# Optimization experiments

Hardware: AMD Instinct MI355X
Metric: run time of the kernel (lower is better)

The kernel has to match this reference:

```python
import jax, jax.numpy as jnp
import numpy as np

B, N, C = 32, 197, 768   # batch, tokens (num_patches+1), emb_dim
KW = 197                 # kw_dim = seq_len
L = 12                   # num_layers (weights shared, norms per-layer)
HID = 3072               # mlp hidden = 4*emb_dim


def layer_norm(x, g, b, eps=1e-5):
    mu = jnp.mean(x, axis=-1, keepdims=True)
    var = jnp.var(x, axis=-1, keepdims=True)
    return (x - mu) * jax.lax.rsqrt(var + eps) * g + b


def attention(x, qkv_w, fc_w, fc_b, ln_g, ln_b, fc2_w, fc2_b, num_heads):
    b, n, c = x.shape
    d = c // num_heads
    qkv = (x @ qkv_w).reshape(b, n, 3, num_heads, d)
    q = qkv[:, :, 0].transpose(0, 2, 1, 3)  # [B,H,N,d]
    k = qkv[:, :, 1].transpose(0, 2, 1, 3)
    v = qkv[:, :, 2].transpose(0, 2, 1, 3)
    scale = d ** -0.5
    attn = jnp.einsum('bhnd,bhmd->bhnm', q, k) * scale      # [B,H,N,N]
    attn = attn @ fc_w + fc_b                                # [B,H,N,KW]
    attn = layer_norm(attn, ln_g, ln_b)
    attn = jax.nn.softmax(attn, axis=-1)
    attn = attn.transpose(0, 1, 3, 2)                        # [B,H,KW,N]
    y = jnp.einsum('bhkn,bhnd->bhkd', attn, v)               # [B,H,KW,d]
    # fc2 applied along KW axis of y.transpose(-2,-1): out[b,h,n,d]
    out = jnp.einsum('bhkd,kn->bnhd', y, fc2_w) + fc2_b[None, :, None, None]
    return out.reshape(b, n, c)


def mlp(x, w1, b1, w2, b2):
    return jax.nn.gelu(x @ w1 + b1, approximate=False) @ w2 + b2


def setup_inputs() -> dict:
    key = jax.random.key(0)
    ks = jax.random.split(key, 16)
    s = 0.02
    return {
        'x': jax.random.normal(ks[0], (B, N, C), jnp.float32),
        'qkv_w': jax.random.normal(ks[1], (C, 3 * C), jnp.float32) * s,
        'fc_w': jax.random.normal(ks[2], (N, KW), jnp.float32) * s,
        'fc_b': jnp.zeros((KW,), jnp.float32),
        'attn_ln_g': jnp.ones((KW,), jnp.float32),
        'attn_ln_b': jnp.zeros((KW,), jnp.float32),
        'fc2_w': jax.random.normal(ks[3], (KW, N), jnp.float32) * s,
        'fc2_b': jnp.zeros((N,), jnp.float32),
        'mlp_w1': jax.random.normal(ks[4], (C, HID), jnp.float32) * s,
        'mlp_b1': jnp.zeros((HID,), jnp.float32),
        'mlp_w2': jax.random.normal(ks[5], (HID, C), jnp.float32) * s,
        'mlp_b2': jnp.zeros((C,), jnp.float32),
        'f_ln_g': jnp.ones((L, C), jnp.float32),
        'f_ln_b': jnp.zeros((L, C), jnp.float32),
        'g_ln_g': jnp.ones((L, C), jnp.float32),
        'g_ln_b': jnp.zeros((L, C), jnp.float32),
        'num_heads': 12,
    }


def reference(x, qkv_w, fc_w, fc_b, attn_ln_g, attn_ln_b, fc2_w, fc2_b,
              mlp_w1, mlp_b1, mlp_w2, mlp_b2, f_ln_g, f_ln_b, g_ln_g, g_ln_b,
              num_heads):
    # x -> cat([x,x]) -> reversible stack -> mean of the two halves
    x1, x2 = x, x
    n_layers = f_ln_g.shape[0]
    for i in range(n_layers):
        # y1 = x1 + f(x2); y2 = x2 + g(y1)  (PreNorm wraps f and g)
        y1 = x1 + attention(layer_norm(x2, f_ln_g[i], f_ln_b[i]),
                            qkv_w, fc_w, fc_b, attn_ln_g, attn_ln_b,
                            fc2_w, fc2_b, num_heads)
        y2 = x2 + mlp(layer_norm(y1, g_ln_g[i], g_ln_b[i]),
                      mlp_w1, mlp_b1, mlp_w2, mlp_b2)
        x1, x2 = y1, y2
    return (x1 + x2) * 0.5
```

## Files before the change

### kernel.cpp

```cpp
#include <hip/hip_runtime.h>
#include <math.h>

#define BB   32
#define NN   197
#define CC   768
#define HH   12
#define DD   64
#define KWW  197
#define HIDD 3072
#define NL   12
#define RR   (BB*NN)
#define BHH  (BB*HH)
#define NP   224

typedef __attribute__((ext_vector_type(8))) short short8;
typedef __attribute__((ext_vector_type(4))) float floatx4;
typedef __attribute__((ext_vector_type(4))) unsigned short us4;

__device__ __forceinline__ unsigned short f2bf(float f) {
    unsigned int u = __float_as_uint(f);
    u += 0x7fff + ((u >> 16) & 1);
    return (unsigned short)(u >> 16);
}

__global__ void ln768_kernel(const float* __restrict__ in, const float* __restrict__ g,
                             const float* __restrict__ be, unsigned short* __restrict__ out) {
    int row = blockIdx.x;
    const float* x = in + (size_t)row * CC;
    unsigned short* o = out + (size_t)row * CC;
    int t = threadIdx.x;
    float v0 = x[t], v1 = x[t+256], v2 = x[t+512];
    float s = v0+v1+v2;
    float q = v0*v0+v1*v1+v2*v2;
    for (int off = 1; off < 64; off <<= 1) {
        s += __shfl_xor(s, off, 64);
        q += __shfl_xor(q, off, 64);
    }
    __shared__ float sh[8];
    int wv = t >> 6, ln = t & 63;
    if (ln == 0) { sh[wv] = s; sh[4+wv] = q; }
    __syncthreads();
    s = sh[0]+sh[1]+sh[2]+sh[3];
    q = sh[4]+sh[5]+sh[6]+sh[7];
    float mu  = s * (1.0f/CC);
    float var = q * (1.0f/CC) - mu*mu;
    float rs  = rsqrtf(var + 1e-5f);
    o[t]     = f2bf((v0-mu)*rs*g[t]     + be[t]);
    o[t+256] = f2bf((v1-mu)*rs*g[t+256] + be[t+256]);
    o[t+512] = f2bf((v2-mu)*rs*g[t+512] + be[t+512]);
}

__global__ void reduce_ln(float* __restrict__ x2, const float* __restrict__ part,
                          const float* __restrict__ b2,
                          const float* __restrict__ g, const float* __restrict__ be,
                          unsigned short* __restrict__ out, int do_ln) {
    int row = blockIdx.x;
    float* xp = x2 + (size_t)row * CC;
    const float* p0 = part + (size_t)row * CC;
    const float* p1 = part + (size_t)RR*CC + (size_t)row * CC;
    int t = threadIdx.x;
    float v0 = xp[t]     + p0[t]     + p1[t]     + b2[t];
    float v1 = xp[t+256] + p0[t+256] + p1[t+256] + b2[t+256];
    float v2 = xp[t+512] + p0[t+512] + p1[t+512] + b2[t+512];
    xp[t] = v0; xp[t+256] = v1; xp[t+512] = v2;
    if (!do_ln) return;
    float s = v0+v1+v2;
    float q = v0*v0+v1*v1+v2*v2;
    for (int off = 1; off < 64; off <<= 1) {
        s += __shfl_xor(s, off, 64);
        q += __shfl_xor(q, off, 64);
    }
    __shared__ float sh[8];
    int wv = t >> 6, ln = t & 63;
    if (ln == 0) { sh[wv] = s; sh[4+wv] = q; }
    __syncthreads();
    s = sh[0]+sh[1]+sh[2]+sh[3];
    q = sh[4]+sh[5]+sh[6]+sh[7];
    float mu  = s * (1.0f/CC);
    float var = q * (1.0f/CC) - mu*mu;
    float rs  = rsqrtf(var + 1e-5f);
    unsigned short* o = out + (size_t)row * CC;
    o[t]     = f2bf((v0-mu)*rs*g[t]     + be[t]);
    o[t+256] = f2bf((v1-mu)*rs*g[t+256] + be[t+256]);
    o[t+512] = f2bf((v2-mu)*rs*g[t+512] + be[t+512]);
}

__global__ void transpose_cast(const float* __restrict__ in, unsigned short* __restrict__ out,
                               int K, int Nd, int Kpad) {
    __shared__ float tile[32][33];
    int n0 = blockIdx.x*32, k0 = blockIdx.y*32;
    int tx = threadIdx.x & 31, ty = threadIdx.x >> 5;
    #pragma unroll
    for (int i = 0; i < 4; i++) {
        int k = k0 + ty + i*8;
        tile[ty + i*8][tx] = (k < K && n0+tx < Nd) ? in[(size_t)k*Nd + n0 + tx] : 0.f;
    }
    __syncthreads();
    #pragma unroll
    for (int i = 0; i < 4; i++) {
        int n = n0 + ty + i*8;
        if (n < Nd && k0 + tx < Kpad) out[(size_t)n*Kpad + k0 + tx] = f2bf(tile[tx][ty + i*8]);
    }
}

template<int EPI, int KS>
__global__ __launch_bounds__(256) void gemm128(
    const unsigned short* __restrict__ A, const unsigned short* __restrict__ Bt,
    const float* __restrict__ bias, float* __restrict__ Cf, unsigned short* __restrict__ Cb,
    int M, int Nd, int K)
{
    __shared__ unsigned short As[128*64];
    __shared__ unsigned short Bs[128*64];
    int tid  = threadIdx.x;
    int wv   = tid >> 6, lane = tid & 63;
    int wm   = wv >> 1, wn = wv & 1;
    int quad = lane >> 4, mrow = lane & 15;
    int rl   = lane >> 3, ps = lane & 7;

    int gx   = gridDim.x;
    int nwg  = gx * gridDim.y;
    int orig = blockIdx.y * gx + blockIdx.x;
    int qq = nwg >> 3, rr = nwg & 7;
    int xcd = orig & 7, idx = orig >> 3;
    int wg  = (xcd < rr ? xcd*(qq+1) : rr*(qq+1) + (xcd-rr)*qq) + idx;
    int bm  = (wg / gx) * 128;
    int bn  = (wg % gx) * 128;

    const int Kc    = K / KS;
    const int kbase = (KS > 1) ? blockIdx.z * Kc : 0;

    floatx4 acc[4][4];
    #pragma unroll
    for (int i = 0; i < 4; i++)
        #pragma unroll
        for (int j = 0; j < 4; j++) acc[i][j] = (floatx4){0.f,0.f,0.f,0.f};

    for (int k0 = kbase; k0 < kbase + Kc; k0 += 64) {
        #pragma unroll
        for (int i = 0; i < 4; i++) {
            int r_ = wv*32 + i*8 + rl;
            int sl = ps ^ (r_ & 7);
            int gr = bm + r_; if (gr > M-1) gr = M-1;
            __builtin_amdgcn_global_load_lds(
                (const __attribute__((address_space(1))) void*)(A + (size_t)gr*K + k0 + sl*8),
                (__attribute__((address_space(3))) void*)(As + (wv*32 + i*8)*64),
                16, 0, 0);
        }
        #pragma unroll
        for (int i = 0; i < 4; i++) {
            int r_ = wv*32 + i*8 + rl;
            int sl = ps ^ (r_ & 7);
            int gr = bn + r_;
            __builtin_amdgcn_global_load_lds(
                (const __attribute__((address_space(1))) void*)(Bt + (size_t)gr*K + k0 + sl*8),
                (__attribute__((address_space(3))) void*)(Bs + (wv*32 + i*8)*64),
                16, 0, 0);
        }
        __syncthreads();
        #pragma unroll
        for (int kk = 0; kk < 2; kk++) {
            short8 af[4], bf[4];
            #pragma unroll
            for (int mi = 0; mi < 4; mi++) {
                int lr = wm*64 + mi*16 + mrow;
                af[mi] = *(const short8*)&As[lr*64 + (((kk<<2)|quad) ^ (lr & 7))*8];
            }
            #pragma unroll
            for (int ni = 0; ni < 4; ni++) {
                int lr = wn*64 + ni*16 + mrow;
                bf[ni] = *(const short8*)&Bs[lr*64 + (((kk<<2)|quad) ^ (lr & 7))*8];
            }
            #pragma unroll
            for (int mi = 0; mi < 4; mi++)
                #pragma unroll
                for (int ni = 0; ni < 4; ni++)
                    acc[mi][ni] = __builtin_amdgcn_mfma_f32_16x16x32_bf16(
                        af[mi], bf[ni], acc[mi][ni], 0, 0, 0);
        }
        __syncthreads();
    }

    float* Cfz = (EPI == 5) ? (Cf + (size_t)blockIdx.z * M * Nd) : Cf;
    #pragma unroll
    for (int mi = 0; mi < 4; mi++) {
        int row0 = bm + wm*64 + mi*16 + quad*4;
        #pragma unroll
        for (int ni = 0; ni < 4; ni++) {
            int col = bn + wn*64 + ni*16 + mrow;
            float bv = (EPI == 2) ? bias[col] : 0.f;
            #pragma unroll
            for (int r = 0; r < 4; r++) {
                int row = row0 + r;
                if (row >= M) continue;
                float v = acc[mi][ni][r] + bv;
                if (EPI == 2) {
                    v = v / (1.0f + __expf(-1.5957691216f*v*(1.0f + 0.044715f*v*v)));
                    Cb[(size_t)row*Nd + col] = f2bf(v);
                } else if (EPI == 5) {
                    Cfz[(size_t)row*Nd + col] = v;
                } else if (EPI == 4) {
                    int sel = col / CC;
                    int rem = col - sel*CC;
                    int h = rem >> 6, d = rem & 63;
                    int b = row / NN, n = row - b*NN;
                    int bh = b*HH + h;
                    unsigned short val = f2bf(v);
                    if (sel < 2)
                        Cb[((size_t)sel*BHH + bh)*NN*DD + (size_t)n*DD + d] = val;
                    else
                        Cb[(size_t)2*BHH*NN*DD + (size_t)bh*DD*NP + (size_t)d*NP + n] = val;
                }
            }
        }
    }
}

__global__ __launch_bounds__(256) void attn_score(
    const unsigned short* __restrict__ qb,
    const unsigned short* __restrict__ kb,
    const unsigned short* __restrict__ fw,
    const float* __restrict__ fbias,
    const float* __restrict__ g, const float* __restrict__ be,
    unsigned short* __restrict__ PT)
{
    int bh = blockIdx.y;
    int bm = blockIdx.x * 64;
    __shared__ unsigned short Ks[224*DD];
    __shared__ unsigned short S1s[64*NP];
    __shared__ unsigned short Bs[224*32];
    __shared__ float gls[NP], bls[NP], bbs[NP];
    int tid = threadIdx.x;
    if (tid < NP) {
        bool vc = tid < KWW;
        gls[tid] = vc ? g[tid]     : 1.f;
        bls[tid] = vc ? be[tid]    : 0.f;
        bbs[tid] = vc ? fbias[tid] : 0.f;
    }
    int wv = tid >> 6, lane = tid & 63;
    int quad = lane >> 4, mrow = lane & 15;

    {
        int lrow = lane >> 3, lko = (lane & 7) * 8;
        #pragma unroll
        for (int i = 0; i < 7; i++) {
            int r = wv*56 + i*8 + lrow;
            __builtin_amdgcn_global_load_lds(
                (const __attribute__((address_space(1))) void*)(kb + ((size_t)bh*NN + r)*DD + lko),
                (__attribute__((address_space(3))) void*)(Ks + (size_t)(wv*56 + i*8)*DD),
                16, 0, 0);
        }
    }
    int qrow = bm + wv*16 + mrow; if (qrow > NN-1) qrow = NN-1;
    short8 aq0 = *(const short8*)&qb[((size_t)bh*NN + qrow)*DD + quad*8];
    short8 aq1 = *(const short8*)&qb[((size_t)bh*NN + qrow)*DD + 32 + quad*8];
    __syncthreads();

    #pragma unroll
    for (int ni = 0; ni < 14; ni++) {
        floatx4 a = (floatx4){0.f,0.f,0.f,0.f};
        short8 bf0 = *(const short8*)&Ks[(size_t)(ni*16 + mrow)*DD + quad*8];
        short8 bf1 = *(const short8*)&Ks[(size_t)(ni*16 + mrow)*DD + 32 + quad*8];
        a = __builtin_amdgcn_mfma_f32_16x16x32_bf16(aq0, bf0, a, 0, 0, 0);
        a = __builtin_amdgcn_mfma_f32_16x16x32_bf16(aq1, bf1, a, 0, 0, 0);
        #pragma unroll
        for (int r = 0; r < 4; r++)
            S1s[(size_t)(wv*16 + quad*4 + r)*NP + ni*16 + mrow] = f2bf(a[r]*0.125f);
    }
    __syncthreads();

    floatx4 acc[14];
    #pragma unroll
    for (int j = 0; j < 14; j++) acc[j] = (floatx4){0.f,0.f,0.f,0.f};
    for (int k0 = 0; k0 < 7; k0++) {
        for (int c = wv; c < 14; c += 4) {
            int gr = c*16 + (lane >> 2); if (gr > KWW-1) gr = KWW-1;
            __builtin_amdgcn_global_load_lds(
                (const __attribute__((address_space(1))) void*)(fw + (size_t)gr*NP + k0*32 + (lane & 3)*8),
                (__attribute__((address_space(3))) void*)(Bs + (size_t)(c*16)*32),
                16, 0, 0);
        }
        __syncthreads();
        short8 af = *(const short8*)&S1s[(size_t)(wv*16 + mrow)*NP + k0*32 + quad*8];
        #pragma unroll
        for (int ni = 0; ni < 14; ni++) {
            short8 bf = *(const short8*)&Bs[(size_t)(ni*16 + mrow)*32 + quad*8];
            acc[ni] = __builtin_amdgcn_mfma_f32_16x16x32_bf16(af, bf, acc[ni], 0, 0, 0);
        }
        __syncthreads();
    }

    float s[4] = {}, q[4] = {};
    #pragma unroll
    for (int ni = 0; ni < 14; ni++) {
        int col = ni*16 + mrow;
        float cm = (col < KWW) ? 1.f : 0.f;
        #pragma unroll
        for (int r = 0; r < 4; r++) {
            float x = acc[ni][r] + bbs[col];
            acc[ni][r] = x;
            s[r] += x*cm; q[r] += x*x*cm;
        }
    }
    #pragma unroll
    for (int o = 1; o < 16; o <<= 1)
        #pragma unroll
        for (int r = 0; r < 4; r++) {
            s[r] += __shfl_xor(s[r], o, 64);
            q[r] += __shfl_xor(q[r], o, 64);
        }
    float mu[4], rs[4], mx[4];
    #pragma unroll
    for (int r = 0; r < 4; r++) {
        mu[r] = s[r] * (1.0f/KWW);
        float var = q[r] * (1.0f/KWW) - mu[r]*mu[r];
        rs[r] = rsqrtf(var + 1e-5f);
        mx[r] = -1e30f;
    }
    #pragma unroll
    for (int ni = 0; ni < 14; ni++) {
        int col = ni*16 + mrow;
        bool vc = col < KWW;
        #pragma unroll
        for (int r = 0; r < 4; r++) {
            float x = (acc[ni][r] - mu[r]) * rs[r] * gls[col] + bls[col];
            acc[ni][r] = x;
            if (vc) mx[r] = fmaxf(mx[r], x);
        }
    }
    #pragma unroll
    for (int o = 1; o < 16; o <<= 1)
        #pragma unroll
        for (int r = 0; r < 4; r++)
            mx[r] = fmaxf(mx[r], __shfl_xor(mx[r], o, 64));
    float se[4] = {};
    #pragma unroll
    for (int ni = 0; ni < 14; ni++) {
        int col = ni*16 + mrow;
        float cm = (col < KWW) ? 1.f : 0.f;
        #pragma unroll
        for (int r = 0; r < 4; r++) {
            float p = __expf(acc[ni][r] - mx[r]) * cm;
            acc[ni][r] = p;
            se[r] += p;
        }
    }
    #pragma unroll
    for (int o = 1; o < 16; o <<= 1)
        #pragma unroll
        for (int r = 0; r < 4; r++)
            se[r] += __shfl_xor(se[r], o, 64);
    unsigned short* Pb = PT + (size_t)bh*NP*NP;
    int row0 = bm + wv*16 + quad*4;
    float inv0 = 1.0f/se[0], inv1 = 1.0f/se[1], inv2 = 1.0f/se[2], inv3 = 1.0f/se[3];
    #pragma unroll
    for (int ni = 0; ni < 14; ni++) {
        int col = ni*16 + mrow;
        if (col >= KWW) continue;
        if (row0 + 3 < NN) {
            us4 o = { f2bf(acc[ni][0]*inv0), f2bf(acc[ni][1]*inv1),
                      f2bf(acc[ni][2]*inv2), f2bf(acc[ni][3]*inv3) };
            *(us4*)&Pb[(size_t)col*NP + row0] = o;
        } else {
            float invs[4] = {inv0, inv1, inv2, inv3};
            #pragma unroll
            for (int r = 0; r < 4; r++)
                if (row0 + r < NN)
                    Pb[(size_t)col*NP + row0 + r] = f2bf(acc[ni][r]*invs[r]);
        }
    }
}

__global__ __launch_bounds__(256) void attn_out2(
    const unsigned short* __restrict__ PT,
    const unsigned short* __restrict__ vT,
    const unsigned short* __restrict__ fw,
    const float* __restrict__ bias,
    float* __restrict__ x1)
{
    int dt = blockIdx.x;
    int bh = blockIdx.y; int b = bh / HH, h = bh - b*HH;
    __shared__ unsigned short yT[16*232];
    int wv = threadIdx.x >> 6, lane = threadIdx.x & 63;
    int quad = lane >> 4, mrow = lane & 15;
    const unsigned short* Pb = PT + (size_t)bh*NP*NP;
    const unsigned short* Vb = vT + (size_t)bh*DD*NP + (size_t)(dt*16)*NP;

    short8 bfv[7];
    #pragma unroll
    for (int kc = 0; kc < 7; kc++)
        bfv[kc] = *(const short8*)&Vb[(size_t)mrow*NP + kc*32 + quad*8];
    #pragma unroll
    for (int i = 0; i < 2; i++) {
        int t0 = wv + i*8, t1 = t0 + 4;
        bool v1 = t1 < 14;
        floatx4 a0 = (floatx4){0.f,0.f,0.f,0.f};
        floatx4 a1 = (floatx4){0.f,0.f,0.f,0.f};
        #pragma unroll
        for (int kc = 0; kc < 7; kc++) {
            short8 p0 = *(const short8*)&Pb[(size_t)(t0*16 + mrow)*NP + kc*32 + quad*8];
            a0 = __builtin_amdgcn_mfma_f32_16x16x32_bf16(p0, bfv[kc], a0, 0, 0, 0);
            if (v1) {
                short8 p1 = *(const short8*)&Pb[(size_t)(t1*16 + mrow)*NP + kc*32 + quad*8];
                a1 = __builtin_amdgcn_mfma_f32_16x16x32_bf16(p1, bfv[kc], a1, 0, 0, 0);
            }
        }
        us4 o0 = { f2bf(a0[0]), f2bf(a0[1]), f2bf(a0[2]), f2bf(a0[3]) };
        *(us4*)&yT[mrow*232 + t0*16 + quad*4] = o0;
        if (v1) {
            us4 o1 = { f2bf(a1[0]), f2bf(a1[1]), f2bf(a1[2]), f2bf(a1[3]) };
            *(us4*)&yT[mrow*232 + t1*16 + quad*4] = o1;
        }
    }
    __syncthreads();

    short8 yf[7];
    #pragma unroll
    for (int kc = 0; kc < 7; kc++)
        yf[kc] = *(const short8*)&yT[mrow*232 + kc*32 + quad*8];
    float* xb = x1 + (size_t)b*NN*CC + (size_t)h*DD + dt*16 + mrow;
    #pragma unroll
    for (int i = 0; i < 2; i++) {
        int n0t = wv + i*8, n1t = n0t + 4;
        bool v1 = n1t < 13;
        floatx4 a0 = (floatx4){0.f,0.f,0.f,0.f};
        floatx4 a1 = (floatx4){0.f,0.f,0.f,0.f};
        #pragma unroll
        for (int kc = 0; kc < 7; kc++) {
            short8 f0 = *(const short8*)&fw[(size_t)(n0t*16 + mrow)*NP + kc*32 + quad*8];
            a0 = __builtin_amdgcn_mfma_f32_16x16x32_bf16(f0, yf[kc], a0, 0, 0, 0);
            if (v1) {
                short8 f1 = *(const short8*)&fw[(size_t)(n1t*16 + mrow)*NP + kc*32 + quad*8];
                a1 = __builtin_amdgcn_mfma_f32_16x16x32_bf16(f1, yf[kc], a1, 0, 0, 0);
            }
        }
        #pragma unroll
        for (int r = 0; r < 4; r++) {
            int n = n0t*16 + quad*4 + r;
            if (n < NN) xb[(size_t)n*CC] += a0[r] + bias[n];
        }
        if (v1) {
            #pragma unroll
            for (int r = 0; r < 4; r++) {
                int n = n1t*16 + quad*4 + r;
                if (n < NN) xb[(size_t)n*CC] += a1[r] + bias[n];
            }
        }
    }
}

__global__ void init_kernel(const float* __restrict__ x, float* __restrict__ x1,
                            float* __restrict__ x2, int n) {
    int i = blockIdx.x*256 + threadIdx.x;
    if (i < n) { float v = x[i]; x1[i] = v; x2[i] = v; }
}
__global__ void final_kernel(const float* __restrict__ x1, const float* __restrict__ x2,
                             float* __restrict__ o, int n) {
    int i = blockIdx.x*256 + threadIdx.x;
    if (i < n) o[i] = 0.5f*(x1[i]+x2[i]);
}

extern "C" void kernel_launch(void* const* d_in, const int* in_sizes, int n_in,
                              void* d_out, int out_size, void* d_ws, size_t ws_size,
                              hipStream_t stream) {
    const float* x     = (const float*)d_in[0];
    const float* qkv_w = (const float*)d_in[1];
    const float* fc_w  = (const float*)d_in[2];
    const float* fc_b  = (const float*)d_in[3];
    const float* alng  = (const float*)d_in[4];
    const float* alnb  = (const float*)d_in[5];
    const float* fc2w  = (const float*)d_in[6];
    const float* fc2b  = (const float*)d_in[7];
    const float* w1    = (const float*)d_in[8];
    const float* b1    = (const float*)d_in[9];
    const float* w2    = (const float*)d_in[10];
    const float* b2    = (const float*)d_in[11];
    const float* flng  = (const float*)d_in[12];
    const float* flnb  = (const float*)d_in[13];
    const float* glng  = (const float*)d_in[14];
    const float* glnb  = (const float*)d_in[15];
    float* out = (float*)d_out;

    float* ws = (float*)d_ws;
    size_t off = 0;
    float* x1 = ws + off; off += (size_t)RR*CC;
    float* x2 = ws + off; off += (size_t)RR*CC;
    float* part = ws + off; off += (size_t)2*RR*CC;
    unsigned short* lnb = (unsigned short*)(ws + off); off += (size_t)RR*CC/2;
    unsigned short* qkvo = (unsigned short*)(ws + off);
    unsigned short* qb = qkvo;
    unsigned short* kb = qkvo + (size_t)BHH*NN*DD;
    unsigned short* vT = qkvo + (size_t)2*BHH*NN*DD;
    off += ((size_t)2*BHH*NN*DD + (size_t)BHH*DD*NP + 1) / 2;
    unsigned short* PT   = (unsigned short*)(ws + off); off += (size_t)BHH*NP*NP/2;
    unsigned short* hid  = (unsigned short*)(ws + off); off += (size_t)RR*HIDD/2;
    unsigned short* qkv_wt = (unsigned short*)(ws + off); off += (size_t)3*CC*CC/2;
    unsigned short* w1t    = (unsigned short*)(ws + off); off += (size_t)CC*HIDD/2;
    unsigned short* w2t    = (unsigned short*)(ws + off); off += (size_t)CC*HIDD/2;
    unsigned short* fc_wt  = (unsigned short*)(ws + off); off += (size_t)NN*NP/2 + 16;
    unsigned short* fc2_wt = (unsigned short*)(ws + off); off += (size_t)NP*NP/2 + 16;

    hipMemsetAsync(vT, 0, (size_t)BHH*DD*NP*2, stream);
    hipMemsetAsync(fc2_wt, 0, (size_t)NP*NP*2, stream);

    transpose_cast<<<dim3(72, 24), 256, 0, stream>>>(qkv_w, qkv_wt, CC, 3*CC, CC);
    transpose_cast<<<dim3(96, 24), 256, 0, stream>>>(w1, w1t, CC, HIDD, CC);
    transpose_cast<<<dim3(24, 96), 256, 0, stream>>>(w2, w2t, HIDD, CC, HIDD);
    transpose_cast<<<dim3(7, 7),   256, 0, stream>>>(fc_w,  fc_wt,  NN, KWW, NP);
    transpose_cast<<<dim3(7, 7),   256, 0, stream>>>(fc2w,  fc2_wt, KWW, NN, NP);

    const int nel = RR*CC;
    init_kernel<<<(nel+255)/256, 256, 0, stream>>>(x, x1, x2, nel);

    const int MT = (RR + 127) / 128;
    ln768_kernel<<<RR, 256, 0, stream>>>(x2, flng, flnb, lnb);
    for (int l = 0; l < NL; l++) {
        gemm128<4,1><<<dim3(3*CC/128, MT), 256, 0, stream>>>(
            lnb, qkv_wt, nullptr, nullptr, qb, RR, 3*CC, CC);
        attn_score<<<dim3(4, BHH), 256, 0, stream>>>(
            qb, kb, fc_wt, fc_b, alng, alnb, PT);
        attn_out2<<<dim3(4, BHH), 256, 0, stream>>>(PT, vT, fc2_wt, fc2b, x1);
        ln768_kernel<<<RR, 256, 0, stream>>>(x1, glng + l*CC, glnb + l*CC, lnb);
        gemm128<2,1><<<dim3(HIDD/128, MT), 256, 0, stream>>>(
            lnb, w1t, b1, nullptr, hid, RR, HIDD, CC);
        gemm128<5,2><<<dim3(CC/128, MT, 2), 256, 0, stream>>>(
            hid, w2t, nullptr, part, nullptr, RR, CC, HIDD);
        reduce_ln<<<RR, 256, 0, stream>>>(
            x2, part, b2, flng + ((l+1 < NL) ? (l+1)*CC : 0),
            flnb + ((l+1 < NL) ? (l+1)*CC : 0), lnb, (l+1 < NL) ? 1 : 0);
    }
    final_kernel<<<(nel+255)/256, 256, 0, stream>>>(x1, x2, out, nel);
}
```

Before: 3.402 ms.

## Double-buffer GEMM LDS tiles and fuse init/final elementwise kernels into LN passes

The 128x128 bf16 GEMM now keeps two LDS stages and issues global-to-LDS loads for the next K tile before running MFMAs on the current one, so memory latency can overlap with compute. LDS use doubles to 64 KB per block, which may lower occupancy. The init copy is merged with the first LayerNorm into one kernel. The final averaging is folded into the last residual reduce kernel, removing two full-tensor passes and two launches.

```diff
diff --git a/kernel.cpp b/kernel.cpp
--- a/kernel.cpp
+++ b/kernel.cpp
@@ -50,10 +50,45 @@
     o[t+512] = f2bf((v2-mu)*rs*g[t+512] + be[t+512]);
 }
 
+__global__ void init_ln(const float* __restrict__ x, float* __restrict__ x1,
+                        float* __restrict__ x2,
+                        const float* __restrict__ g, const float* __restrict__ be,
+                        unsigned short* __restrict__ out) {
+    int row = blockIdx.x;
+    const float* xp = x + (size_t)row * CC;
+    int t = threadIdx.x;
+    float v0 = xp[t], v1 = xp[t+256], v2 = xp[t+512];
+    float* a = x1 + (size_t)row * CC;
+    float* b = x2 + (size_t)row * CC;
+    a[t] = v0; a[t+256] = v1; a[t+512] = v2;
+    b[t] = v0; b[t+256] = v1; b[t+512] = v2;
+    float s = v0+v1+v2;
+    float q = v0*v0+v1*v1+v2*v2;
+    for (int off = 1; off < 64; off <<= 1) {
+        s += __shfl_xor(s, off, 64);
+        q += __shfl_xor(q, off, 64);
+    }
+    __shared__ float sh[8];
+    int wv = t >> 6, ln = t & 63;
+    if (ln == 0) { sh[wv] = s; sh[4+wv] = q; }
+    __syncthreads();
+    s = sh[0]+sh[1]+sh[2]+sh[3];
+    q = sh[4]+sh[5]+sh[6]+sh[7];
+    float mu  = s * (1.0f/CC);
+    float var = q * (1.0f/CC) - mu*mu;
+    float rs  = rsqrtf(var + 1e-5f);
+    unsigned short* o = out + (size_t)row * CC;
+    o[t]     = f2bf((v0-mu)*rs*g[t]     + be[t]);
+    o[t+256] = f2bf((v1-mu)*rs*g[t+256] + be[t+256]);
+    o[t+512] = f2bf((v2-mu)*rs*g[t+512] + be[t+512]);
+}
+
 __global__ void reduce_ln(float* __restrict__ x2, const float* __restrict__ part,
                           const float* __restrict__ b2,
                           const float* __restrict__ g, const float* __restrict__ be,
-                          unsigned short* __restrict__ out, int do_ln) {
+                          unsigned short* __restrict__ out,
+                          const float* __restrict__ x1f, float* __restrict__ outf,
+                          int mode) {
     int row = blockIdx.x;
     float* xp = x2 + (size_t)row * CC;
     const float* p0 = part + (size_t)row * CC;
@@ -63,7 +98,14 @@
     float v1 = xp[t+256] + p0[t+256] + p1[t+256] + b2[t+256];
     float v2 = xp[t+512] + p0[t+512] + p1[t+512] + b2[t+512];
     xp[t] = v0; xp[t+256] = v1; xp[t+512] = v2;
-    if (!do_ln) return;
+    if (mode == 2) {
+        const float* xo = x1f + (size_t)row * CC;
+        float* o = outf + (size_t)row * CC;
+        o[t]     = 0.5f*(xo[t]     + v0);
+        o[t+256] = 0.5f*(xo[t+256] + v1);
+        o[t+512] = 0.5f*(xo[t+512] + v2);
+        return;
+    }
     float s = v0+v1+v2;
     float q = v0*v0+v1*v1+v2*v2;
     for (int off = 1; off < 64; off <<= 1) {
@@ -109,8 +151,8 @@
     const float* __restrict__ bias, float* __restrict__ Cf, unsigned short* __restrict__ Cb,
     int M, int Nd, int K)
 {
-    __shared__ unsigned short As[128*64];
-    __shared__ unsigned short Bs[128*64];
+    __shared__ unsigned short As[2*128*64];
+    __shared__ unsigned short Bs[2*128*64];
     int tid  = threadIdx.x;
     int wv   = tid >> 6, lane = tid & 63;
     int wm   = wv >> 1, wn = wv & 1;
@@ -128,6 +170,7 @@
 
     const int Kc    = K / KS;
     const int kbase = (KS > 1) ? blockIdx.z * Kc : 0;
+    const int nt    = Kc / 64;
 
     floatx4 acc[4][4];
     #pragma unroll
@@ -135,40 +178,49 @@
         #pragma unroll
         for (int j = 0; j < 4; j++) acc[i][j] = (floatx4){0.f,0.f,0.f,0.f};
 
-    for (int k0 = kbase; k0 < kbase + Kc; k0 += 64) {
-        #pragma unroll
-        for (int i = 0; i < 4; i++) {
-            int r_ = wv*32 + i*8 + rl;
-            int sl = ps ^ (r_ & 7);
-            int gr = bm + r_; if (gr > M-1) gr = M-1;
-            __builtin_amdgcn_global_load_lds(
-                (const __attribute__((address_space(1))) void*)(A + (size_t)gr*K + k0 + sl*8),
-                (__attribute__((address_space(3))) void*)(As + (wv*32 + i*8)*64),
-                16, 0, 0);
-        }
-        #pragma unroll
-        for (int i = 0; i < 4; i++) {
-            int r_ = wv*32 + i*8 + rl;
-            int sl = ps ^ (r_ & 7);
-            int gr = bn + r_;
-            __builtin_amdgcn_global_load_lds(
-                (const __attribute__((address_space(1))) void*)(Bt + (size_t)gr*K + k0 + sl*8),
-                (__attribute__((address_space(3))) void*)(Bs + (wv*32 + i*8)*64),
-                16, 0, 0);
-        }
-        __syncthreads();
+#define G128_STAGE(buf, kcol)                                                     \
+    do {                                                                          \
+        _Pragma("unroll")                                                         \
+        for (int i_ = 0; i_ < 4; i_++) {                                          \
+            int r_ = wv*32 + i_*8 + rl;                                           \
+            int sl_ = ps ^ (r_ & 7);                                              \
+            int gr_ = bm + r_; if (gr_ > M-1) gr_ = M-1;                          \
+            __builtin_amdgcn_global_load_lds(                                     \
+                (const __attribute__((address_space(1))) void*)(A + (size_t)gr_*K + (kcol) + sl_*8), \
+                (__attribute__((address_space(3))) void*)(As + (buf)*8192 + (wv*32 + i_*8)*64), \
+                16, 0, 0);                                                        \
+        }                                                                         \
+        _Pragma("unroll")                                                         \
+        for (int i_ = 0; i_ < 4; i_++) {                                          \
+            int r_ = wv*32 + i_*8 + rl;                                           \
+            int sl_ = ps ^ (r_ & 7);                                              \
+            int gr_ = bn + r_;                                                    \
+            __builtin_amdgcn_global_load_lds(                                     \
+                (const __attribute__((address_space(1))) void*)(Bt + (size_t)gr_*K + (kcol) + sl_*8), \
+                (__attribute__((address_space(3))) void*)(Bs + (buf)*8192 + (wv*32 + i_*8)*64), \
+                16, 0, 0);                                                        \
+        }                                                                         \
+    } while (0)
+
+    G128_STAGE(0, kbase);
+    __syncthreads();
+
+    for (int t = 0; t < nt; ++t) {
+        const int c = t & 1;
+        if (t + 1 < nt) G128_STAGE(c ^ 1, kbase + (t+1)*64);
+        const int cb = c * 8192;
         #pragma unroll
         for (int kk = 0; kk < 2; kk++) {
             short8 af[4], bf[4];
             #pragma unroll
             for (int mi = 0; mi < 4; mi++) {
                 int lr = wm*64 + mi*16 + mrow;
-                af[mi] = *(const short8*)&As[lr*64 + (((kk<<2)|quad) ^ (lr & 7))*8];
+                af[mi] = *(const short8*)&As[cb + lr*64 + (((kk<<2)|quad) ^ (lr & 7))*8];
             }
             #pragma unroll
             for (int ni = 0; ni < 4; ni++) {
                 int lr = wn*64 + ni*16 + mrow;
-                bf[ni] = *(const short8*)&Bs[lr*64 + (((kk<<2)|quad) ^ (lr & 7))*8];
+                bf[ni] = *(const short8*)&Bs[cb + lr*64 + (((kk<<2)|quad) ^ (lr & 7))*8];
             }
             #pragma unroll
             for (int mi = 0; mi < 4; mi++)
@@ -179,6 +231,7 @@
         }
         __syncthreads();
     }
+#undef G128_STAGE
 
     float* Cfz = (EPI == 5) ? (Cf + (size_t)blockIdx.z * M * Nd) : Cf;
     #pragma unroll
@@ -448,17 +501,6 @@
     }
 }
 
-__global__ void init_kernel(const float* __restrict__ x, float* __restrict__ x1,
-                            float* __restrict__ x2, int n) {
-    int i = blockIdx.x*256 + threadIdx.x;
-    if (i < n) { float v = x[i]; x1[i] = v; x2[i] = v; }
-}
-__global__ void final_kernel(const float* __restrict__ x1, const float* __restrict__ x2,
-                             float* __restrict__ o, int n) {
-    int i = blockIdx.x*256 + threadIdx.x;
-    if (i < n) o[i] = 0.5f*(x1[i]+x2[i]);
-}
-
 extern "C" void kernel_launch(void* const* d_in, const int* in_sizes, int n_in,
                               void* d_out, int out_size, void* d_ws, size_t ws_size,
                               hipStream_t stream) {
@@ -508,11 +550,9 @@
     transpose_cast<<<dim3(7, 7),   256, 0, stream>>>(fc_w,  fc_wt,  NN, KWW, NP);
     transpose_cast<<<dim3(7, 7),   256, 0, stream>>>(fc2w,  fc2_wt, KWW, NN, NP);
 
-    const int nel = RR*CC;
-    init_kernel<<<(nel+255)/256, 256, 0, stream>>>(x, x1, x2, nel);
+    init_ln<<<RR, 256, 0, stream>>>(x, x1, x2, flng, flnb, lnb);
 
     const int MT = (RR + 127) / 128;
-    ln768_kernel<<<RR, 256, 0, stream>>>(x2, flng, flnb, lnb);
     for (int l = 0; l < NL; l++) {
         gemm128<4,1><<<dim3(3*CC/128, MT), 256, 0, stream>>>(
             lnb, qkv_wt, nullptr, nullptr, qb, RR, 3*CC, CC);
@@ -524,9 +564,13 @@
             lnb, w1t, b1, nullptr, hid, RR, HIDD, CC);
         gemm128<5,2><<<dim3(CC/128, MT, 2), 256, 0, stream>>>(
             hid, w2t, nullptr, part, nullptr, RR, CC, HIDD);
-        reduce_ln<<<RR, 256, 0, stream>>>(
-            x2, part, b2, flng + ((l+1 < NL) ? (l+1)*CC : 0),
-            flnb + ((l+1 < NL) ? (l+1)*CC : 0), lnb, (l+1 < NL) ? 1 : 0);
-    }
-    final_kernel<<<(nel+255)/256, 256, 0, stream>>>(x1, x2, out, nel);
-}
+        if (l + 1 < NL) {
+            reduce_ln<<<RR, 256, 0, stream>>>(
+                x2, part, b2, flng + (l+1)*CC, flnb + (l+1)*CC, lnb,
+                nullptr, nullptr, 1);
+        } else {
+            reduce_ln<<<RR, 256, 0, stream>>>(
+                x2, part, b2, nullptr, nullptr, nullptr, x1, out, 2);
+        }
+    }
+}
```

Result: slower. 3.624 ms (+6.5%).
